# Performance work log

Measured on AMD Instinct MI355X. Metric: run time of the kernel, lower is better.

Reference implementation:

```python
import jax, jax.numpy as jnp
import numpy as np

N = 1_000_000
NUM_CLASSES = 80
ALPHA = 0.25
GAMMA = 2.0
CENTER_W = 0.1
EPS = 1e-7  # torchvision generalized_box_iou_loss eps


def _make_boxes(u):
    # u: [N,4] uniform in [0,1) -> valid xyxy boxes inside ~1024x1024 canvas
    x1 = u[:, 0] * 1024.0
    y1 = u[:, 1] * 1024.0
    x2 = x1 + u[:, 2] * 256.0 + 1.0
    y2 = y1 + u[:, 3] * 256.0 + 1.0
    return jnp.stack([x1, y1, x2, y2], axis=-1)


def setup_inputs() -> dict:
    key = jax.random.key(0)
    k1, k2, k3, k4, k5 = jax.random.split(key, 5)
    cls_logits = jax.random.normal(k1, (N, NUM_CLASSES), dtype=jnp.float32)
    bbox_reg = _make_boxes(jax.random.uniform(k2, (N, 4), dtype=jnp.float32))
    centerness = jax.random.normal(k3, (N,), dtype=jnp.float32)
    gt_bboxes = _make_boxes(jax.random.uniform(k4, (N, 4), dtype=jnp.float32))
    gt_classes = jax.random.randint(k5, (N,), 0, NUM_CLASSES, dtype=jnp.int32)
    return {"cls_logits": cls_logits, "bbox_reg": bbox_reg,
            "centerness": centerness, "gt_bboxes": gt_bboxes,
            "gt_classes": gt_classes}


def _giou_loss_mean(pred, gt):
    # elementwise pairwise GIoU loss, mean reduction (torchvision semantics)
    px1, py1, px2, py2 = pred[:, 0], pred[:, 1], pred[:, 2], pred[:, 3]
    gx1, gy1, gx2, gy2 = gt[:, 0], gt[:, 1], gt[:, 2], gt[:, 3]
    iw = jnp.clip(jnp.minimum(px2, gx2) - jnp.maximum(px1, gx1), 0.0)
    ih = jnp.clip(jnp.minimum(py2, gy2) - jnp.maximum(py1, gy1), 0.0)
    inter = iw * ih
    area_p = (px2 - px1) * (py2 - py1)
    area_g = (gx2 - gx1) * (gy2 - gy1)
    union = area_p + area_g - inter
    iou = inter / (union + EPS)
    cw = jnp.maximum(px2, gx2) - jnp.minimum(px1, gx1)
    ch = jnp.maximum(py2, gy2) - jnp.minimum(py1, gy1)
    area_c = cw * ch
    giou = iou - (area_c - union) / (area_c + EPS)
    return jnp.mean(1.0 - giou)


def reference(cls_logits, bbox_reg, centerness, gt_bboxes, gt_classes):
    # focal loss built from standard cross-entropy (as in the torch module)
    logp = jax.nn.log_softmax(cls_logits, axis=-1)            # [N, C]
    ce = -jnp.take_along_axis(logp, gt_classes[:, None].astype(jnp.int32), axis=1)[:, 0]
    pt = jnp.exp(-ce)
    focal_loss = jnp.mean(ALPHA * (1.0 - pt) ** GAMMA * ce)

    iou_loss = _giou_loss_mean(bbox_reg, gt_bboxes)

    # BCE-with-logits vs all-ones target: mean(softplus(-x))
    center_loss = jnp.mean(jnp.logaddexp(0.0, -centerness))

    total = focal_loss + iou_loss + CENTER_W * center_loss
    return total, focal_loss, iou_loss, center_loss
```

## Files before the change

### kernel.cpp

```cpp
#include <hip/hip_runtime.h>
#include <math.h>

#define NUM_CLASSES 80
#define F4_PER_ROW  20
#define ROWS_PER_BLOCK 128
#define THREADS 128
#define ROW_STRIDE 84

constexpr float ALPHA = 0.25f;
constexpr float CENTER_W = 0.1f;
constexpr float EPS_GIOU = 1e-7f;

__global__ __launch_bounds__(THREADS) void hdm_loss_kernel(
    const float* __restrict__ cls_logits,
    const float* __restrict__ bbox_reg,
    const float* __restrict__ centerness,
    const float* __restrict__ gt_bboxes,
    const int*   __restrict__ gt_classes,
    double* __restrict__ partials,
    int n)
{
    __shared__ float tile[ROWS_PER_BLOCK * ROW_STRIDE];

    const int t = threadIdx.x;
    const int row_base = blockIdx.x * ROWS_PER_BLOCK;
    const int row = row_base + t;

    const int total_f4 = n * F4_PER_ROW;
    const int slab_base = row_base * F4_PER_ROW;
    const float4* src = (const float4*)cls_logits;
    #pragma unroll
    for (int k = 0; k < F4_PER_ROW; ++k) {
        const int F = k * THREADS + t;
        const int gF = slab_base + F;
        if (gF < total_f4) {
            const float4 v = src[gF];
            const int lrow = F / F4_PER_ROW;
            const int c4   = F % F4_PER_ROW;
            *(float4*)&tile[lrow * ROW_STRIDE + c4 * 4] = v;
        }
    }
    __syncthreads();

    float focal_t = 0.0f, giou_t = 0.0f, center_t = 0.0f;

    if (row < n) {
        const float4* myrow = (const float4*)&tile[t * ROW_STRIDE];
        float m = -INFINITY;
        #pragma unroll
        for (int j = 0; j < F4_PER_ROW; ++j) {
            const float4 v = myrow[j];
            m = fmaxf(m, fmaxf(fmaxf(v.x, v.y), fmaxf(v.z, v.w)));
        }
        float s = 0.0f;
        #pragma unroll
        for (int j = 0; j < F4_PER_ROW; ++j) {
            const float4 v = myrow[j];
            s += __expf(v.x - m);
            s += __expf(v.y - m);
            s += __expf(v.z - m);
            s += __expf(v.w - m);
        }
        const int gc = gt_classes[row];
        const float xg = tile[t * ROW_STRIDE + gc];
        const float lse = m + __logf(s);
        const float ce  = lse - xg;
        const float pt  = __expf(-ce);
        const float omp = 1.0f - pt;
        focal_t = ALPHA * omp * omp * ce;

        const float4 p = ((const float4*)bbox_reg)[row];
        const float4 g = ((const float4*)gt_bboxes)[row];
        const float iw = fmaxf(fminf(p.z, g.z) - fmaxf(p.x, g.x), 0.0f);
        const float ih = fmaxf(fminf(p.w, g.w) - fmaxf(p.y, g.y), 0.0f);
        const float inter  = iw * ih;
        const float area_p = (p.z - p.x) * (p.w - p.y);
        const float area_g = (g.z - g.x) * (g.w - g.y);
        const float uni    = area_p + area_g - inter;
        const float iou    = inter / (uni + EPS_GIOU);
        const float cw = fmaxf(p.z, g.z) - fminf(p.x, g.x);
        const float ch = fmaxf(p.w, g.w) - fminf(p.y, g.y);
        const float area_c = cw * ch;
        const float giou = iou - (area_c - uni) / (area_c + EPS_GIOU);
        giou_t = 1.0f - giou;

        const float c = centerness[row];
        center_t = fmaxf(-c, 0.0f) + log1pf(__expf(-fabsf(c)));
    }

    double f = (double)focal_t, gi = (double)giou_t, ce_ = (double)center_t;
    #pragma unroll
    for (int off = 32; off > 0; off >>= 1) {
        f   += __shfl_down(f,   off, 64);
        gi  += __shfl_down(gi,  off, 64);
        ce_ += __shfl_down(ce_, off, 64);
    }
    __shared__ double sf[2], sg[2], sc[2];
    const int lane = t & 63;
    const int wave = t >> 6;
    if (lane == 0) { sf[wave] = f; sg[wave] = gi; sc[wave] = ce_; }
    __syncthreads();
    if (t == 0) {
        partials[blockIdx.x * 3 + 0] = sf[0] + sf[1];
        partials[blockIdx.x * 3 + 1] = sg[0] + sg[1];
        partials[blockIdx.x * 3 + 2] = sc[0] + sc[1];
    }
}

__global__ __launch_bounds__(256) void hdm_finalize_kernel(
    const double* __restrict__ partials, int nblocks, int n,
    float* __restrict__ out)
{
    double f = 0.0, g = 0.0, c = 0.0;
    for (int i = threadIdx.x; i < nblocks; i += 256) {
        f += partials[i * 3 + 0];
        g += partials[i * 3 + 1];
        c += partials[i * 3 + 2];
    }
    #pragma unroll
    for (int off = 32; off > 0; off >>= 1) {
        f += __shfl_down(f, off, 64);
        g += __shfl_down(g, off, 64);
        c += __shfl_down(c, off, 64);
    }
    __shared__ double sf[4], sg[4], sc[4];
    const int lane = threadIdx.x & 63;
    const int wave = threadIdx.x >> 6;
    if (lane == 0) { sf[wave] = f; sg[wave] = g; sc[wave] = c; }
    __syncthreads();
    if (threadIdx.x == 0) {
        double tf = 0.0, tg = 0.0, tc = 0.0;
        #pragma unroll
        for (int w = 0; w < 4; ++w) { tf += sf[w]; tg += sg[w]; tc += sc[w]; }
        const double inv_n = 1.0 / (double)n;
        const double focal_mean  = tf * inv_n;
        const double iou_mean    = tg * inv_n;
        const double center_mean = tc * inv_n;
        const double total = focal_mean + iou_mean + (double)CENTER_W * center_mean;
        out[0] = (float)total;
        out[1] = (float)focal_mean;
        out[2] = (float)iou_mean;
        out[3] = (float)center_mean;
    }
}

extern "C" void kernel_launch(void* const* d_in, const int* in_sizes, int n_in,
                              void* d_out, int out_size, void* d_ws, size_t ws_size,
                              hipStream_t stream) {
    const float* cls_logits = (const float*)d_in[0];
    const float* bbox_reg   = (const float*)d_in[1];
    const float* centerness = (const float*)d_in[2];
    const float* gt_bboxes  = (const float*)d_in[3];
    const int*   gt_classes = (const int*)d_in[4];
    float* out = (float*)d_out;

    const int n = in_sizes[2];
    const int nblocks = (n + ROWS_PER_BLOCK - 1) / ROWS_PER_BLOCK;
    double* partials = (double*)d_ws;

    hdm_loss_kernel<<<nblocks, THREADS, 0, stream>>>(
        cls_logits, bbox_reg, centerness, gt_bboxes, gt_classes, partials, n);
    hdm_finalize_kernel<<<1, 256, 0, stream>>>(partials, nblocks, n, out);
}
```

Before: 515.5 us.

## Split each softmax row across four threads with shuffle reductions

Blocks now hold 64 rows with 256 threads, and four lanes cooperate on each row. Each lane handles 20 logits and combines max and sum-exp through xor shuffles. The three loss terms are spread across lanes 0, 1 and 2 of each row group. Global loads are issued into registers before the LDS stores so more memory requests are in flight. This targets per-thread serial exp work and low memory-level parallelism, at the cost of twice as many blocks, twice as many partials for the finalize pass, and idle lanes in the epilogue.

```diff
diff --git a/kernel.cpp b/kernel.cpp
--- a/kernel.cpp
+++ b/kernel.cpp
@@ -3,8 +3,10 @@
 
 #define NUM_CLASSES 80
 #define F4_PER_ROW  20
-#define ROWS_PER_BLOCK 128
-#define THREADS 128
+#define ROWS_PER_BLOCK 64
+#define THREADS 256
+#define F4_PER_SLAB (ROWS_PER_BLOCK * F4_PER_ROW)
+#define F4_PER_THREAD (F4_PER_SLAB / THREADS)
 #define ROW_STRIDE 84
 
 constexpr float ALPHA = 0.25f;
@@ -24,51 +26,64 @@
 
     const int t = threadIdx.x;
     const int row_base = blockIdx.x * ROWS_PER_BLOCK;
-    const int row = row_base + t;
 
     const int total_f4 = n * F4_PER_ROW;
     const int slab_base = row_base * F4_PER_ROW;
     const float4* src = (const float4*)cls_logits;
+    float4 v[F4_PER_THREAD];
     #pragma unroll
-    for (int k = 0; k < F4_PER_ROW; ++k) {
+    for (int k = 0; k < F4_PER_THREAD; ++k) {
+        const int gF = slab_base + k * THREADS + t;
+        v[k] = (gF < total_f4) ? src[gF] : make_float4(0.f, 0.f, 0.f, 0.f);
+    }
+    #pragma unroll
+    for (int k = 0; k < F4_PER_THREAD; ++k) {
         const int F = k * THREADS + t;
-        const int gF = slab_base + F;
-        if (gF < total_f4) {
-            const float4 v = src[gF];
-            const int lrow = F / F4_PER_ROW;
-            const int c4   = F % F4_PER_ROW;
-            *(float4*)&tile[lrow * ROW_STRIDE + c4 * 4] = v;
-        }
+        const int lrow = F / F4_PER_ROW;
+        const int c4   = F % F4_PER_ROW;
+        *(float4*)&tile[lrow * ROW_STRIDE + c4 * 4] = v[k];
     }
     __syncthreads();
 
+    const int lrow = t >> 2;
+    const int q    = t & 3;
+    const int row  = row_base + lrow;
+    const bool live = (row < n);
+
+    float4 w[5];
+    const float4* myseg = (const float4*)&tile[lrow * ROW_STRIDE + q * 20];
+    #pragma unroll
+    for (int j = 0; j < 5; ++j) w[j] = myseg[j];
+
+    float m = -INFINITY;
+    #pragma unroll
+    for (int j = 0; j < 5; ++j)
+        m = fmaxf(m, fmaxf(fmaxf(w[j].x, w[j].y), fmaxf(w[j].z, w[j].w)));
+    m = fmaxf(m, __shfl_xor(m, 1, 64));
+    m = fmaxf(m, __shfl_xor(m, 2, 64));
+
+    float s = 0.0f;
+    #pragma unroll
+    for (int j = 0; j < 5; ++j) {
+        s += __expf(w[j].x - m);
+        s += __expf(w[j].y - m);
+        s += __expf(w[j].z - m);
+        s += __expf(w[j].w - m);
+    }
+    s += __shfl_xor(s, 1, 64);
+    s += __shfl_xor(s, 2, 64);
+
     float focal_t = 0.0f, giou_t = 0.0f, center_t = 0.0f;
 
-    if (row < n) {
-        const float4* myrow = (const float4*)&tile[t * ROW_STRIDE];
-        float m = -INFINITY;
-        #pragma unroll
-        for (int j = 0; j < F4_PER_ROW; ++j) {
-            const float4 v = myrow[j];
-            m = fmaxf(m, fmaxf(fmaxf(v.x, v.y), fmaxf(v.z, v.w)));
-        }
-        float s = 0.0f;
-        #pragma unroll
-        for (int j = 0; j < F4_PER_ROW; ++j) {
-            const float4 v = myrow[j];
-            s += __expf(v.x - m);
-            s += __expf(v.y - m);
-            s += __expf(v.z - m);
-            s += __expf(v.w - m);
-        }
+    if (live && q == 0) {
         const int gc = gt_classes[row];
-        const float xg = tile[t * ROW_STRIDE + gc];
+        const float xg = tile[lrow * ROW_STRIDE + gc];
         const float lse = m + __logf(s);
         const float ce  = lse - xg;
         const float pt  = __expf(-ce);
         const float omp = 1.0f - pt;
         focal_t = ALPHA * omp * omp * ce;
-
+    } else if (live && q == 1) {
         const float4 p = ((const float4*)bbox_reg)[row];
         const float4 g = ((const float4*)gt_bboxes)[row];
         const float iw = fmaxf(fminf(p.z, g.z) - fmaxf(p.x, g.x), 0.0f);
@@ -83,7 +98,7 @@
         const float area_c = cw * ch;
         const float giou = iou - (area_c - uni) / (area_c + EPS_GIOU);
         giou_t = 1.0f - giou;
-
+    } else if (live && q == 2) {
         const float c = centerness[row];
         center_t = fmaxf(-c, 0.0f) + log1pf(__expf(-fabsf(c)));
     }
@@ -95,15 +110,15 @@
         gi  += __shfl_down(gi,  off, 64);
         ce_ += __shfl_down(ce_, off, 64);
     }
-    __shared__ double sf[2], sg[2], sc[2];
+    __shared__ double sf[4], sg[4], sc[4];
     const int lane = t & 63;
     const int wave = t >> 6;
     if (lane == 0) { sf[wave] = f; sg[wave] = gi; sc[wave] = ce_; }
     __syncthreads();
     if (t == 0) {
-        partials[blockIdx.x * 3 + 0] = sf[0] + sf[1];
-        partials[blockIdx.x * 3 + 1] = sg[0] + sg[1];
-        partials[blockIdx.x * 3 + 2] = sc[0] + sc[1];
+        partials[blockIdx.x * 3 + 0] = sf[0] + sf[1] + sf[2] + sf[3];
+        partials[blockIdx.x * 3 + 1] = sg[0] + sg[1] + sg[2] + sg[3];
+        partials[blockIdx.x * 3 + 2] = sc[0] + sc[1] + sc[2] + sc[3];
     }
 }
 
```

Result: faster. 463.4 us (-10.1%).
